# Optimization experiments

Hardware: AMD Instinct MI355X
Metric: run time of the kernel (lower is better)

## Reference

```python
import jax, jax.numpy as jnp
import numpy as np

EPS = 1e-6
B, T, D = 8, 4096, 512


def setup_inputs() -> dict:
    key = jax.random.key(0)
    ks = jax.random.split(key, 8)
    s = 1.0 / np.sqrt(D)
    return {
        "summarization": jax.random.normal(ks[0], (B, D), jnp.float32),
        "decoder_output": jax.random.normal(ks[1], (B, T, D), jnp.float32),
        "W_hist": jax.random.normal(ks[2], (D, D), jnp.float32) * s,
        "b_hist": jnp.zeros((D,), jnp.float32),
        "W1": jax.random.normal(ks[3], (D, D), jnp.float32) * s,
        "W2": jax.random.normal(ks[4], (D, D), jnp.float32) * s,
        "W_out": jax.random.normal(ks[5], (D, D), jnp.float32) * s,
        "b_out": jnp.zeros((D,), jnp.float32),
        "gamma": jnp.ones((D,), jnp.float32),
        "beta": jnp.zeros((D,), jnp.float32),
    }


def reference(summarization, decoder_output, W_hist, b_hist, W1, W2, W_out, b_out, gamma, beta):
    # Causal running mean: equivalent to tril-mask bmm / row-count, but O(T).
    tgt_len = decoder_output.shape[1]
    counts = jnp.arange(1, tgt_len + 1, dtype=decoder_output.dtype)[None, :, None]
    history = jnp.cumsum(decoder_output, axis=1) / counts            # [B,T,D]
    history = jnp.tanh(history @ W_hist + b_hist)                    # history_linear + tanh
    # TransformMinus: linear1(summ) - linear2(history), then linear_out + tanh
    summ_proj = (summarization @ W1)[:, None, :]                     # [B,1,D] broadcasts over T
    out = summ_proj - history @ W2
    future = jnp.tanh(out @ W_out + b_out)
    # LayerPostprocessing (eval: dropout = identity): LayerNorm(future + decoder_output)
    x = future + decoder_output
    mu = jnp.mean(x, axis=-1, keepdims=True)
    var = jnp.mean(jnp.square(x - mu), axis=-1, keepdims=True)
    return (x - mu) / jnp.sqrt(var + EPS) * gamma + beta
```

## Files before the change

kernel.cpp:

```cpp
#include <hip/hip_runtime.h>
#include <hip/hip_bf16.h>
#include <stdint.h>
#include <stddef.h>

#define DEV static __device__ __forceinline__

typedef __attribute__((ext_vector_type(8))) short short8;
typedef __attribute__((ext_vector_type(4))) float floatx4;

constexpr int Tn = 4096, Dn = 512;
constexpr int NC = 128, CTm = 32;

union U8s { uint4 u4; unsigned short us[8]; };
union U4f { float4 f4; float f[4]; };
union U4s { uint2 u2; unsigned short us[4]; };

DEV float b2f(unsigned short u) {
  union { unsigned int i; float f; } c; c.i = ((unsigned int)u) << 16; return c.f;
}
DEV unsigned short f2b(float f) {
  union { float f; unsigned int u; } c; c.f = f;
  unsigned int r = c.u + 0x7fffu + ((c.u >> 16) & 1u);
  return (unsigned short)(r >> 16);
}
DEV float fast_tanh(float x) {
  float e = __expf(2.0f * x);
  return 1.0f - 2.0f / (e + 1.0f);
}

typedef __attribute__((address_space(1))) void GVOID;
typedef __attribute__((address_space(3))) void LVOID;
DEV void async16(const unsigned short* g, unsigned short* l) {
  __builtin_amdgcn_global_load_lds((GVOID*)g, (LVOID*)l, 16, 0, 0);
}

__global__ void k_fuse1(const float* __restrict__ dec, float* __restrict__ part,
                        const float* __restrict__ Wh, const float* __restrict__ Wo,
                        const float* __restrict__ W1, const float* __restrict__ W2,
                        unsigned short* __restrict__ WhT, unsigned short* __restrict__ WoT,
                        unsigned short* __restrict__ W1b, unsigned short* __restrict__ W2b) {
  int blk = blockIdx.x;
  if (blk < 512) {
    int idx = blk * 256 + threadIdx.x;
    int d4 = idx & 127;
    int c  = (idx >> 7) & (NC - 1);
    int b  = idx >> 14;
    const float* p = dec + ((size_t)b * Tn + (size_t)c * CTm) * Dn + d4 * 4;
    float s[4] = {0,0,0,0};
#pragma unroll 4
    for (int i = 0; i < CTm; ++i) {
      U4f v; v.f4 = *(const float4*)(p + (size_t)i * Dn);
#pragma unroll
      for (int j = 0; j < 4; ++j) s[j] += v.f[j];
    }
    float* o = part + ((size_t)(b * NC + c)) * Dn + d4 * 4;
#pragma unroll
    for (int j = 0; j < 4; ++j) o[j] = s[j];
  } else {
    int wb = blk - 512;
    if (wb < 128) {
      const float* in = (wb < 64) ? Wh : Wo;
      unsigned short* out = (wb < 64) ? WhT : WoT;
      int lb = wb & 63;
      __shared__ float t[64][65];
      int n0 = (lb & 7) * 64, k0 = (lb >> 3) * 64;
#pragma unroll
      for (int l = 0; l < 16; ++l) {
        int lin = l * 256 + threadIdx.x;
        int r = lin >> 6, c = lin & 63;
        t[r][c] = in[(size_t)(k0 + r) * 512 + n0 + c];
      }
      __syncthreads();
#pragma unroll
      for (int l = 0; l < 16; ++l) {
        int lin = l * 256 + threadIdx.x;
        int r = lin >> 6, c = lin & 63;
        out[(size_t)(n0 + r) * 512 + k0 + c] = f2b(t[c][r]);
      }
    } else {
      const float* in = (wb < 160) ? W1 : W2;
      unsigned short* out = (wb < 160) ? W1b : W2b;
      int lb = (wb - 128) & 31;
      size_t base = ((size_t)lb * 256 + threadIdx.x) * 32;
#pragma unroll
      for (int l = 0; l < 8; ++l) {
        U4f v; v.f4 = *(const float4*)(in + base + l * 4);
        U4s o;
#pragma unroll
        for (int j = 0; j < 4; ++j) o.us[j] = f2b(v.f[j]);
        *(uint2*)(out + base + l * 4) = o.u2;
      }
    }
  }
}

__global__ __launch_bounds__(256, 2)
void k_gemmH(const unsigned short* __restrict__ A, const unsigned short* __restrict__ BT,
             unsigned short* __restrict__ C, const float* __restrict__ bias) {
  __shared__ alignas(16) unsigned short sA[128 * 64];
  __shared__ alignas(16) unsigned short sB[128 * 64];
  const int m0 = blockIdx.x * 128, n0 = blockIdx.y * 128;
  const int tid  = threadIdx.x;
  const int lane = tid & 63;
  const int w    = tid >> 6;
  const int wm   = (w >> 1) * 64;
  const int wn   = (w & 1) * 64;
  const int rs   = lane & 15;
  const int quad = lane >> 4;

  floatx4 acc[4][4];
#pragma unroll
  for (int i = 0; i < 4; ++i)
#pragma unroll
    for (int j = 0; j < 4; ++j) acc[i][j] = (floatx4){0.f, 0.f, 0.f, 0.f};

  for (int kt = 0; kt < 512; kt += 64) {
#pragma unroll
    for (int l = 0; l < 4; ++l) {
      int ch = l * 256 + tid;
      int r = ch >> 3, kc = ch & 7;
      async16(A  + (size_t)(m0 + r) * 512 + kt + kc * 8, sA + (size_t)ch * 8);
      async16(BT + (size_t)(n0 + r) * 512 + kt + kc * 8, sB + (size_t)ch * 8);
    }
    asm volatile("s_waitcnt vmcnt(0)" ::: "memory");
    __syncthreads();

#pragma unroll
    for (int kk = 0; kk < 2; ++kk) {
      const int kb = kk * 32 + quad * 8;
      short8 af[4], bfr[4];
#pragma unroll
      for (int i = 0; i < 4; ++i)
        af[i] = *(const short8*)(sA + (size_t)(wm + i * 16 + rs) * 64 + kb);
#pragma unroll
      for (int j = 0; j < 4; ++j)
        bfr[j] = *(const short8*)(sB + (size_t)(wn + j * 16 + rs) * 64 + kb);
#pragma unroll
      for (int i = 0; i < 4; ++i)
#pragma unroll
        for (int j = 0; j < 4; ++j)
          acc[i][j] = __builtin_amdgcn_mfma_f32_16x16x32_bf16(af[i], bfr[j], acc[i][j], 0, 0, 0);
    }
    __syncthreads();
  }

#pragma unroll
  for (int i = 0; i < 4; ++i) {
#pragma unroll
    for (int j = 0; j < 4; ++j) {
      const int colg = n0 + wn + j * 16 + rs;
#pragma unroll
      for (int r = 0; r < 4; ++r) {
        const int rowg = m0 + wm + i * 16 + quad * 4 + r;
        C[(size_t)rowg * 512 + colg] = f2b(fast_tanh(acc[i][j][r] + bias[colg]));
      }
    }
  }
}

template<int EPI>
DEV void gemm64_core(const unsigned short* __restrict__ A,
                     const unsigned short* __restrict__ BT,
                     unsigned short* __restrict__ C,
                     const float* __restrict__ spo,
                     const float* __restrict__ dec,
                     const float* __restrict__ gamma,
                     const float* __restrict__ beta,
                     float* __restrict__ out,
                     int m0) {
  __shared__ alignas(16) unsigned short sA[64 * 32];
  __shared__ alignas(16) unsigned short sB[512 * 32];
  __shared__ float lnS[64][4];
  __shared__ float lnQ[64][4];
  const int tid  = threadIdx.x;
  const int lane = tid & 63;
  const int w    = tid >> 6;
  const int wr   = w >> 2;
  const int wc   = w & 3;
  const int rs   = lane & 15;
  const int quad = lane >> 4;

  floatx4 acc[2][8];
#pragma unroll
  for (int i = 0; i < 2; ++i)
#pragma unroll
    for (int j = 0; j < 8; ++j) acc[i][j] = (floatx4){0.f, 0.f, 0.f, 0.f};

  for (int t = 0; t < 16; ++t) {
    const int kt = t * 32;
    if (tid < 256) {
      int r = tid >> 2, c = tid & 3;
      int kc = (c ^ ((r >> 1) & 3)) * 8;
      async16(A + (size_t)(m0 + r) * 512 + kt + kc, &sA[tid * 8]);
    }
#pragma unroll
    for (int l = 0; l < 4; ++l) {
      int ch = l * 512 + tid;
      int r = ch >> 2, c = ch & 3;
      int kc = (c ^ ((r >> 1) & 3)) * 8;
      async16(BT + (size_t)r * 512 + kt + kc, &sB[ch * 8]);
    }
    asm volatile("s_waitcnt vmcnt(0)" ::: "memory");
    __syncthreads();

    const int co = (quad ^ ((rs >> 1) & 3)) * 8;
    short8 af0 = *(const short8*)(&sA[(wr * 32 + rs) * 32 + co]);
    short8 af1 = *(const short8*)(&sA[(wr * 32 + 16 + rs) * 32 + co]);
#pragma unroll
    for (int nj = 0; nj < 8; ++nj) {
      short8 bf = *(const short8*)(&sB[(wc * 128 + nj * 16 + rs) * 32 + co]);
      acc[0][nj] = __builtin_amdgcn_mfma_f32_16x16x32_bf16(af0, bf, acc[0][nj], 0, 0, 0);
      acc[1][nj] = __builtin_amdgcn_mfma_f32_16x16x32_bf16(af1, bf, acc[1][nj], 0, 0, 0);
    }
    __syncthreads();
  }

  if constexpr (EPI == 2) {
#pragma unroll
    for (int nj = 0; nj < 8; ++nj) {
      const int colg = wc * 128 + nj * 16 + rs;
#pragma unroll
      for (int mi = 0; mi < 2; ++mi) {
#pragma unroll
        for (int r = 0; r < 4; ++r) {
          const int rowg = m0 + wr * 32 + mi * 16 + quad * 4 + r;
          C[(size_t)rowg * 512 + colg] = f2b(acc[mi][nj][r]);
        }
      }
    }
  } else {
    const int bidx = m0 >> 12;
#pragma unroll
    for (int mi = 0; mi < 2; ++mi) {
#pragma unroll
      for (int r = 0; r < 4; ++r) {
        const int lrow = wr * 32 + mi * 16 + quad * 4 + r;
        const size_t rowg = (size_t)(m0 + lrow);
        float s = 0.f, sq = 0.f;
#pragma unroll
        for (int nj = 0; nj < 8; ++nj) {
          const int colg = wc * 128 + nj * 16 + rs;
          float sp = spo[bidx * Dn + colg];
          float dv = dec[rowg * 512 + colg];
          float xf = fast_tanh(sp - acc[mi][nj][r]) + dv;
          acc[mi][nj][r] = xf;
          s += xf; sq += xf * xf;
        }
#pragma unroll
        for (int o = 8; o > 0; o >>= 1) { s += __shfl_xor(s, o, 64); sq += __shfl_xor(sq, o, 64); }
        if (rs == 0) { lnS[lrow][wc] = s; lnQ[lrow][wc] = sq; }
      }
    }
    __syncthreads();
#pragma unroll
    for (int mi = 0; mi < 2; ++mi) {
#pragma unroll
      for (int r = 0; r < 4; ++r) {
        const int lrow = wr * 32 + mi * 16 + quad * 4 + r;
        const size_t rowg = (size_t)(m0 + lrow);
        float s = 0.f, sq = 0.f;
#pragma unroll
        for (int k = 0; k < 4; ++k) { s += lnS[lrow][k]; sq += lnQ[lrow][k]; }
        float mu   = s * (1.0f / 512.0f);
        float var  = sq * (1.0f / 512.0f) - mu * mu;
        float rstd = rsqrtf(var + 1e-6f);
#pragma unroll
        for (int nj = 0; nj < 8; ++nj) {
          const int colg = wc * 128 + nj * 16 + rs;
          out[rowg * 512 + colg] = (acc[mi][nj][r] - mu) * rstd * gamma[colg] + beta[colg];
        }
      }
    }
  }
}

__global__ __launch_bounds__(512, 4)
void k_gemmFLN(const unsigned short* __restrict__ A, const unsigned short* __restrict__ BT,
               const float* __restrict__ spo, const float* __restrict__ dec,
               const float* __restrict__ gamma, const float* __restrict__ beta,
               float* __restrict__ out) {
  gemm64_core<5>(A, BT, nullptr, spo, dec, gamma, beta, out, blockIdx.x * 64);
}

__global__ __launch_bounds__(512, 4)
void k_wgemm2(const unsigned short* __restrict__ WoT,
              const unsigned short* __restrict__ W2b, const unsigned short* __restrict__ W1b,
              unsigned short* __restrict__ W2WoT, unsigned short* __restrict__ W1WoT,
              float* __restrict__ part) {
  int blk = blockIdx.x;
  if (blk < 16) {
    const unsigned short* BT = (blk & 8) ? W1b : W2b;
    unsigned short* Cc = (blk & 8) ? W1WoT : W2WoT;
    gemm64_core<2>(WoT, BT, Cc, nullptr, nullptr, nullptr, nullptr, nullptr,
                   (blk & 7) * 64);
  } else {
    int idx = (blk - 16) * 512 + threadIdx.x;
    int d4 = idx & 127;
    int b  = idx >> 7;
    float* p = part + (size_t)b * NC * Dn + d4 * 4;
    float s[4] = {0, 0, 0, 0};
    for (int c0 = 0; c0 < NC; c0 += 8) {
      U4f v[8];
#pragma unroll
      for (int i = 0; i < 8; ++i) v[i].f4 = *(const float4*)(p + (size_t)(c0 + i) * Dn);
#pragma unroll
      for (int i = 0; i < 8; ++i) {
        U4f o;
#pragma unroll
        for (int j = 0; j < 4; ++j) { o.f[j] = s[j]; s[j] += v[i].f[j]; }
        *(float4*)(p + (size_t)(c0 + i) * Dn) = o.f4;
      }
    }
  }
}

__global__ void k_fuse3(const float* __restrict__ dec, const float* __restrict__ part,
                        unsigned short* __restrict__ M,
                        const float* __restrict__ summ,
                        const unsigned short* __restrict__ W1WoT,
                        const float* __restrict__ bo, float* __restrict__ spo) {
  int blk = blockIdx.x;
  if (blk < 512) {
    int idx = blk * 256 + threadIdx.x;
    int d4 = idx & 127;
    int c  = (idx >> 7) & (NC - 1);
    int b  = idx >> 14;
    size_t rbase = (size_t)b * Tn + (size_t)c * CTm;
    U4f s; s.f4 = *(const float4*)(part + ((size_t)b * NC + c) * Dn + d4 * 4);
    int t0 = c * CTm;
    const float* dp = dec + rbase * Dn + d4 * 4;
    unsigned short* mp = M + rbase * Dn + d4 * 4;
#pragma unroll 4
    for (int i = 0; i < CTm; ++i) {
      U4f v; v.f4 = *(const float4*)(dp + (size_t)i * Dn);
      float inv = 1.0f / (float)(t0 + i + 1);
      U4s o;
#pragma unroll
      for (int j = 0; j < 4; ++j) { s.f[j] += v.f[j]; o.us[j] = f2b(s.f[j] * inv); }
      *(uint2*)(mp + (size_t)i * Dn) = o.u2;
    }
  } else {
    int widx = (blk - 512) * 4 + (threadIdx.x >> 6);
    int lane = threadIdx.x & 63;
    int n = widx & 511; int b = widx >> 9;
    U8s w8; w8.u4 = *(const uint4*)(W1WoT + (size_t)n * Dn + lane * 8);
    U4f s0, s1;
    s0.f4 = *(const float4*)(summ + (size_t)b * Dn + lane * 8);
    s1.f4 = *(const float4*)(summ + (size_t)b * Dn + lane * 8 + 4);
    float acc = 0.f;
#pragma unroll
    for (int j = 0; j < 4; ++j) acc += s0.f[j] * b2f(w8.us[j]);
#pragma unroll
    for (int j = 0; j < 4; ++j) acc += s1.f[j] * b2f(w8.us[j + 4]);
#pragma unroll
    for (int o = 32; o > 0; o >>= 1) acc += __shfl_xor(acc, o, 64);
    if (lane == 0) spo[(size_t)b * Dn + n] = acc + bo[n];
  }
}

extern "C" void kernel_launch(void* const* d_in, const int* in_sizes, int n_in,
                              void* d_out, int out_size, void* d_ws, size_t ws_size,
                              hipStream_t stream) {
  (void)in_sizes; (void)n_in; (void)out_size; (void)ws_size;
  const float* summ = (const float*)d_in[0];
  const float* dec  = (const float*)d_in[1];
  const float* Wh   = (const float*)d_in[2];
  const float* bh   = (const float*)d_in[3];
  const float* W1   = (const float*)d_in[4];
  const float* W2   = (const float*)d_in[5];
  const float* Wo   = (const float*)d_in[6];
  const float* bo   = (const float*)d_in[7];
  const float* gam  = (const float*)d_in[8];
  const float* bet  = (const float*)d_in[9];
  float* out = (float*)d_out;

  char* ws = (char*)d_ws;
  unsigned short* Mbuf  = (unsigned short*)(ws);
  unsigned short* Hbuf  = (unsigned short*)(ws + 33554432);
  float*          part  = (float*)(ws + 67108864);
  float*          spo   = (float*)(ws + 69206016);
  unsigned short* WhT   = (unsigned short*)(ws + 69238784);
  unsigned short* WoT   = (unsigned short*)(ws + 69763072);
  unsigned short* W2b   = (unsigned short*)(ws + 70287360);
  unsigned short* W2WoT = (unsigned short*)(ws + 70811648);
  unsigned short* W1b   = (unsigned short*)(ws + 71335936);
  unsigned short* W1WoT = (unsigned short*)(ws + 71860224);

  k_fuse1<<<704, 256, 0, stream>>>(dec, part, Wh, Wo, W1, W2, WhT, WoT, W1b, W2b);

  k_wgemm2<<<18, 512, 0, stream>>>(WoT, W2b, W1b, W2WoT, W1WoT, part);

  k_fuse3<<<1536, 256, 0, stream>>>(dec, part, Mbuf, summ, W1WoT, bo, spo);

  k_gemmH<<<dim3(256, 4), 256, 0, stream>>>(Mbuf, WhT, Hbuf, bh);

  k_gemmFLN<<<512, 512, 0, stream>>>(Hbuf, W2WoT, spo, dec, gam, bet, out);
}
```

Baseline: 234.8 us.

## Double-buffer full-width GEMM core with 1024-thread blocks for both big GEMMs

Replaces the 128x128 tiled history GEMM and the 64-row full-width FLN GEMM with one shared full-width core using 128-row tiles, 1024 threads and double-buffered LDS stages. Loads for the next K slice are issued before computing the current one, with partial vmcnt waits and raw barriers, and MFMA sections get raised wave priority. The aim is to overlap global-to-LDS traffic with MFMA work and to reuse each B tile across more rows. In exchange, LDS use per block roughly doubles and blocks get much larger, which lowers occupancy. The hand-counted vmcnt values also have to match exactly the number of async loads each wave issues.

```diff
diff --git a/kernel.cpp b/kernel.cpp
--- a/kernel.cpp
+++ b/kernel.cpp
@@ -94,84 +94,21 @@
   }
 }
 
-__global__ __launch_bounds__(256, 2)
-void k_gemmH(const unsigned short* __restrict__ A, const unsigned short* __restrict__ BT,
-             unsigned short* __restrict__ C, const float* __restrict__ bias) {
-  __shared__ alignas(16) unsigned short sA[128 * 64];
-  __shared__ alignas(16) unsigned short sB[128 * 64];
-  const int m0 = blockIdx.x * 128, n0 = blockIdx.y * 128;
-  const int tid  = threadIdx.x;
-  const int lane = tid & 63;
-  const int w    = tid >> 6;
-  const int wm   = (w >> 1) * 64;
-  const int wn   = (w & 1) * 64;
-  const int rs   = lane & 15;
-  const int quad = lane >> 4;
-
-  floatx4 acc[4][4];
-#pragma unroll
-  for (int i = 0; i < 4; ++i)
-#pragma unroll
-    for (int j = 0; j < 4; ++j) acc[i][j] = (floatx4){0.f, 0.f, 0.f, 0.f};
-
-  for (int kt = 0; kt < 512; kt += 64) {
-#pragma unroll
-    for (int l = 0; l < 4; ++l) {
-      int ch = l * 256 + tid;
-      int r = ch >> 3, kc = ch & 7;
-      async16(A  + (size_t)(m0 + r) * 512 + kt + kc * 8, sA + (size_t)ch * 8);
-      async16(BT + (size_t)(n0 + r) * 512 + kt + kc * 8, sB + (size_t)ch * 8);
-    }
-    asm volatile("s_waitcnt vmcnt(0)" ::: "memory");
-    __syncthreads();
-
-#pragma unroll
-    for (int kk = 0; kk < 2; ++kk) {
-      const int kb = kk * 32 + quad * 8;
-      short8 af[4], bfr[4];
-#pragma unroll
-      for (int i = 0; i < 4; ++i)
-        af[i] = *(const short8*)(sA + (size_t)(wm + i * 16 + rs) * 64 + kb);
-#pragma unroll
-      for (int j = 0; j < 4; ++j)
-        bfr[j] = *(const short8*)(sB + (size_t)(wn + j * 16 + rs) * 64 + kb);
-#pragma unroll
-      for (int i = 0; i < 4; ++i)
-#pragma unroll
-        for (int j = 0; j < 4; ++j)
-          acc[i][j] = __builtin_amdgcn_mfma_f32_16x16x32_bf16(af[i], bfr[j], acc[i][j], 0, 0, 0);
-    }
-    __syncthreads();
-  }
-
-#pragma unroll
-  for (int i = 0; i < 4; ++i) {
-#pragma unroll
-    for (int j = 0; j < 4; ++j) {
-      const int colg = n0 + wn + j * 16 + rs;
-#pragma unroll
-      for (int r = 0; r < 4; ++r) {
-        const int rowg = m0 + wm + i * 16 + quad * 4 + r;
-        C[(size_t)rowg * 512 + colg] = f2b(fast_tanh(acc[i][j][r] + bias[colg]));
-      }
-    }
-  }
-}
-
 template<int EPI>
-DEV void gemm64_core(const unsigned short* __restrict__ A,
+DEV void gemmFW_core(const unsigned short* __restrict__ A,
                      const unsigned short* __restrict__ BT,
                      unsigned short* __restrict__ C,
+                     const float* __restrict__ bias,
                      const float* __restrict__ spo,
                      const float* __restrict__ dec,
                      const float* __restrict__ gamma,
                      const float* __restrict__ beta,
                      float* __restrict__ out,
                      int m0) {
-  __shared__ alignas(16) unsigned short sA[64 * 32];
-  __shared__ alignas(16) unsigned short sB[512 * 32];
-  __shared__ float lnS[64][4];
-  __shared__ float lnQ[64][4];
+  __shared__ alignas(16) unsigned short sA[2][128 * 32];
+  __shared__ alignas(16) unsigned short sB[2][512 * 32];
+  __shared__ float lnS[128][4];
+  __shared__ float lnQ[128][4];
   const int tid  = threadIdx.x;
   const int lane = tid & 63;
   const int w    = tid >> 6;
@@ -186,45 +123,57 @@
 #pragma unroll
     for (int j = 0; j < 8; ++j) acc[i][j] = (floatx4){0.f, 0.f, 0.f, 0.f};
 
-  for (int t = 0; t < 16; ++t) {
-    const int kt = t * 32;
-    if (tid < 256) {
+  auto STAGE = [&](int kt, int buf) {
+    if (tid < 512) {
       int r = tid >> 2, c = tid & 3;
       int kc = (c ^ ((r >> 1) & 3)) * 8;
-      async16(A + (size_t)(m0 + r) * 512 + kt + kc, &sA[tid * 8]);
-    }
-#pragma unroll
-    for (int l = 0; l < 4; ++l) {
-      int ch = l * 512 + tid;
+      async16(A + (size_t)(m0 + r) * 512 + kt + kc, &sA[buf][tid * 8]);
+    }
+#pragma unroll
+    for (int l = 0; l < 2; ++l) {
+      int ch = l * 1024 + tid;
       int r = ch >> 2, c = ch & 3;
       int kc = (c ^ ((r >> 1) & 3)) * 8;
-      async16(BT + (size_t)r * 512 + kt + kc, &sB[ch * 8]);
-    }
-    asm volatile("s_waitcnt vmcnt(0)" ::: "memory");
-    __syncthreads();
-
+      async16(BT + (size_t)r * 512 + kt + kc, &sB[buf][ch * 8]);
+    }
+  };
+
+  auto COMPUTE = [&](int buf) {
+    __builtin_amdgcn_s_setprio(1);
     const int co = (quad ^ ((rs >> 1) & 3)) * 8;
-    short8 af0 = *(const short8*)(&sA[(wr * 32 + rs) * 32 + co]);
-    short8 af1 = *(const short8*)(&sA[(wr * 32 + 16 + rs) * 32 + co]);
+    short8 af0 = *(const short8*)(&sA[buf][(wr * 32 + rs) * 32 + co]);
+    short8 af1 = *(const short8*)(&sA[buf][(wr * 32 + 16 + rs) * 32 + co]);
 #pragma unroll
     for (int nj = 0; nj < 8; ++nj) {
-      short8 bf = *(const short8*)(&sB[(wc * 128 + nj * 16 + rs) * 32 + co]);
+      short8 bf = *(const short8*)(&sB[buf][(wc * 128 + nj * 16 + rs) * 32 + co]);
       acc[0][nj] = __builtin_amdgcn_mfma_f32_16x16x32_bf16(af0, bf, acc[0][nj], 0, 0, 0);
       acc[1][nj] = __builtin_amdgcn_mfma_f32_16x16x32_bf16(af1, bf, acc[1][nj], 0, 0, 0);
     }
-    __syncthreads();
-  }
-
-  if constexpr (EPI == 2) {
+    __builtin_amdgcn_s_setprio(0);
+  };
+
+  STAGE(0, 0);
+  for (int t = 0; t < 15; ++t) {
+    STAGE((t + 1) * 32, (t + 1) & 1);
+    if (w < 8) asm volatile("s_waitcnt vmcnt(3)\n\ts_barrier" ::: "memory");
+    else       asm volatile("s_waitcnt vmcnt(2)\n\ts_barrier" ::: "memory");
+    COMPUTE(t & 1);
+    asm volatile("s_barrier" ::: "memory");
+  }
+  asm volatile("s_waitcnt vmcnt(0)\n\ts_barrier" ::: "memory");
+  COMPUTE(1);
+
+  if constexpr (EPI == 0) {
 #pragma unroll
     for (int nj = 0; nj < 8; ++nj) {
       const int colg = wc * 128 + nj * 16 + rs;
+      float bb = bias[colg];
 #pragma unroll
       for (int mi = 0; mi < 2; ++mi) {
 #pragma unroll
         for (int r = 0; r < 4; ++r) {
           const int rowg = m0 + wr * 32 + mi * 16 + quad * 4 + r;
-          C[(size_t)rowg * 512 + colg] = f2b(acc[mi][nj][r]);
+          C[(size_t)rowg * 512 + colg] = f2b(fast_tanh(acc[mi][nj][r] + bb));
         }
       }
     }
@@ -274,12 +223,82 @@
   }
 }
 
-__global__ __launch_bounds__(512, 4)
+__global__ __launch_bounds__(1024)
+void k_gemmH(const unsigned short* __restrict__ A, const unsigned short* __restrict__ BT,
+             unsigned short* __restrict__ C, const float* __restrict__ bias) {
+  gemmFW_core<0>(A, BT, C, bias, nullptr, nullptr, nullptr, nullptr, nullptr,
+                 blockIdx.x * 128);
+}
+
+__global__ __launch_bounds__(1024)
 void k_gemmFLN(const unsigned short* __restrict__ A, const unsigned short* __restrict__ BT,
                const float* __restrict__ spo, const float* __restrict__ dec,
                const float* __restrict__ gamma, const float* __restrict__ beta,
                float* __restrict__ out) {
-  gemm64_core<5>(A, BT, nullptr, spo, dec, gamma, beta, out, blockIdx.x * 64);
+  gemmFW_core<5>(A, BT, nullptr, nullptr, spo, dec, gamma, beta, out,
+                 blockIdx.x * 128);
+}
+
+DEV void gemm64_core(const unsigned short* __restrict__ A,
+                     const unsigned short* __restrict__ BT,
+                     unsigned short* __restrict__ C, int m0) {
+  __shared__ alignas(16) unsigned short sA[64 * 32];
+  __shared__ alignas(16) unsigned short sB[512 * 32];
+  const int tid  = threadIdx.x;
+  const int lane = tid & 63;
+  const int w    = tid >> 6;
+  const int wr   = w >> 2;
+  const int wc   = w & 3;
+  const int rs   = lane & 15;
+  const int quad = lane >> 4;
+
+  floatx4 acc[2][8];
+#pragma unroll
+  for (int i = 0; i < 2; ++i)
+#pragma unroll
+    for (int j = 0; j < 8; ++j) acc[i][j] = (floatx4){0.f, 0.f, 0.f, 0.f};
+
+  for (int t = 0; t < 16; ++t) {
+    const int kt = t * 32;
+    if (tid < 256) {
+      int r = tid >> 2, c = tid & 3;
+      int kc = (c ^ ((r >> 1) & 3)) * 8;
+      async16(A + (size_t)(m0 + r) * 512 + kt + kc, &sA[tid * 8]);
+    }
+#pragma unroll
+    for (int l = 0; l < 4; ++l) {
+      int ch = l * 512 + tid;
+      int r = ch >> 2, c = ch & 3;
+      int kc = (c ^ ((r >> 1) & 3)) * 8;
+      async16(BT + (size_t)r * 512 + kt + kc, &sB[ch * 8]);
+    }
+    asm volatile("s_waitcnt vmcnt(0)" ::: "memory");
+    __syncthreads();
+
+    const int co = (quad ^ ((rs >> 1) & 3)) * 8;
+    short8 af0 = *(const short8*)(&sA[(wr * 32 + rs) * 32 + co]);
+    short8 af1 = *(const short8*)(&sA[(wr * 32 + 16 + rs) * 32 + co]);
+#pragma unroll
+    for (int nj = 0; nj < 8; ++nj) {
+      short8 bf = *(const short8*)(&sB[(wc * 128 + nj * 16 + rs) * 32 + co]);
+      acc[0][nj] = __builtin_amdgcn_mfma_f32_16x16x32_bf16(af0, bf, acc[0][nj], 0, 0, 0);
+      acc[1][nj] = __builtin_amdgcn_mfma_f32_16x16x32_bf16(af1, bf, acc[1][nj], 0, 0, 0);
+    }
+    __syncthreads();
+  }
+
+#pragma unroll
+  for (int nj = 0; nj < 8; ++nj) {
+    const int colg = wc * 128 + nj * 16 + rs;
+#pragma unroll
+    for (int mi = 0; mi < 2; ++mi) {
+#pragma unroll
+      for (int r = 0; r < 4; ++r) {
+        const int rowg = m0 + wr * 32 + mi * 16 + quad * 4 + r;
+        C[(size_t)rowg * 512 + colg] = f2b(acc[mi][nj][r]);
+      }
+    }
+  }
 }
 
 __global__ __launch_bounds__(512, 4)
@@ -291,8 +310,7 @@
   if (blk < 16) {
     const unsigned short* BT = (blk & 8) ? W1b : W2b;
     unsigned short* Cc = (blk & 8) ? W1WoT : W2WoT;
-    gemm64_core<2>(WoT, BT, Cc, nullptr, nullptr, nullptr, nullptr, nullptr,
-                   (blk & 7) * 64);
+    gemm64_core(WoT, BT, Cc, (blk & 7) * 64);
   } else {
     int idx = (blk - 16) * 512 + threadIdx.x;
     int d4 = idx & 127;
@@ -392,7 +410,7 @@
 
   k_fuse3<<<1536, 256, 0, stream>>>(dec, part, Mbuf, summ, W1WoT, bo, spo);
 
-  k_gemmH<<<dim3(256, 4), 256, 0, stream>>>(Mbuf, WhT, Hbuf, bh);
-
-  k_gemmFLN<<<512, 512, 0, stream>>>(Hbuf, W2WoT, spo, dec, gam, bet, out);
-}
+  k_gemmH<<<256, 1024, 0, stream>>>(Mbuf, WhT, Hbuf, bh);
+
+  k_gemmFLN<<<256, 1024, 0, stream>>>(Hbuf, W2WoT, spo, dec, gam, bet, out);
+}
```

Measured after the change: 231.5 us. Within noise of the previous version (-1.4%).
